# Optimization experiments

Measured on AMD Instinct MI355X. Metric: run time of the kernel, lower is better.

Reference implementation:

```python
import jax, jax.numpy as jnp
import numpy as np

B, L, D = 4, 2048, 1024
H, DK, DV = 16, 64, 64
EPS = 1e-6


def setup_inputs() -> dict:
    key = jax.random.key(0)
    ks = jax.random.split(key, 8)
    s = 0.02
    return {
        "q": jax.random.normal(ks[0], (B, L, D), dtype=jnp.float32),
        "k": jax.random.normal(ks[1], (B, L, D), dtype=jnp.float32),
        "v": jax.random.normal(ks[2], (B, L, D), dtype=jnp.float32),
        "Wq": jax.random.normal(ks[3], (H * DK, D), dtype=jnp.float32) * s,
        "Wk": jax.random.normal(ks[4], (H * DK, D), dtype=jnp.float32) * s,
        "Wv": jax.random.normal(ks[5], (H * DV, D), dtype=jnp.float32) * s,
        "Wfc": jax.random.normal(ks[6], (D, H * DV), dtype=jnp.float32) * s,
        "ln_g": jnp.ones((D,), dtype=jnp.float32),
        "ln_b": jnp.zeros((D,), dtype=jnp.float32),
    }


def reference(q, k, v, Wq, Wk, Wv, Wfc, ln_g, ln_b):
    residual = q
    # projections (Linear: x @ W.T), reshape to [B, H, L, d]
    qh = (q @ Wq.T).reshape(B, L, H, DK).transpose(0, 2, 1, 3)
    kh = (k @ Wk.T).reshape(B, L, H, DK).transpose(0, 2, 1, 3)
    vh = (v @ Wv.T).reshape(B, L, H, DV).transpose(0, 2, 1, 3)
    temperature = jnp.float32(DK) ** 0.5
    # scores [B, H, Lq, Lk]
    scores = jnp.einsum("bhqd,bhkd->bhqk", qh / temperature, kh)
    attn = jax.nn.softmax(scores, axis=-1)
    ctx = jnp.einsum("bhqk,bhkd->bhqd", attn, vh)  # [B, H, L, DV]
    ctx = ctx.transpose(0, 2, 1, 3).reshape(B, L, H * DV)
    out = ctx @ Wfc.T + residual
    # LayerNorm(eps=1e-6)
    mu = jnp.mean(out, axis=-1, keepdims=True)
    var = jnp.var(out, axis=-1, keepdims=True)
    out = (out - mu) * jax.lax.rsqrt(var + EPS) * ln_g + ln_b
    return out, attn
```

## Files before the change

### kernel.cpp

```cpp
#include <hip/hip_runtime.h>
#include <hip/hip_bf16.h>

typedef __bf16 bf16;
typedef __bf16 bf16x8 __attribute__((ext_vector_type(8)));
typedef __bf16 bf16x4 __attribute__((ext_vector_type(4)));
typedef __bf16 bf16x2 __attribute__((ext_vector_type(2)));
typedef float f32x4 __attribute__((ext_vector_type(4)));
typedef float f32x16 __attribute__((ext_vector_type(16)));
typedef unsigned int u32x4 __attribute__((ext_vector_type(4)));

#define MFMA_BF16(a, b, c) __builtin_amdgcn_mfma_f32_16x16x32_bf16((a), (b), (c), 0, 0, 0)
#define MFMA32(a, b, c) __builtin_amdgcn_mfma_f32_32x32x16_bf16((a), (b), (c), 0, 0, 0)

#if defined(__has_builtin)
#if __has_builtin(__builtin_amdgcn_exp2f)
#define EXP2F(x) __builtin_amdgcn_exp2f(x)
#endif
#endif
#ifndef EXP2F
#define EXP2F(x) exp2f(x)
#endif

static constexpr int Bc = 4, Lc = 2048, Dc = 1024, Hc = 16, DKc = 64;
static constexpr int BLc = Bc * Lc;
static constexpr float CEXP = 0.18033688011112042f;

__device__ inline unsigned pk2(float a, float b) {
  bf16x2 t;
  t[0] = (bf16)a;
  t[1] = (bf16)b;
  return __builtin_bit_cast(unsigned, t);
}

__global__ __launch_bounds__(256) void cvt_all(const float* __restrict__ s0,
                                               const float* __restrict__ s1,
                                               const float* __restrict__ s2,
                                               const float* __restrict__ s3,
                                               bf16* __restrict__ dst) {
  size_t i = ((size_t)blockIdx.x * 256 + threadIdx.x) * 8;
  const float* srcs[4] = {s0, s1, s2, s3};
  const float* sp = srcs[i >> 20] + (i & 1048575);
  float4 f0 = ((const float4*)sp)[0];
  float4 f1 = ((const float4*)sp)[1];
  bf16x8 o;
  o[0] = (bf16)f0.x; o[1] = (bf16)f0.y; o[2] = (bf16)f0.z; o[3] = (bf16)f0.w;
  o[4] = (bf16)f1.x; o[5] = (bf16)f1.y; o[6] = (bf16)f1.z; o[7] = (bf16)f1.w;
  *(bf16x8*)(dst + i) = o;
}

__global__ __launch_bounds__(256) void qkv_gemm(const float* __restrict__ qin,
                                                const float* __restrict__ kin,
                                                const float* __restrict__ vin,
                                                const bf16* __restrict__ Wb,
                                                bf16* __restrict__ qh,
                                                bf16* __restrict__ kh,
                                                bf16* __restrict__ vt) {
  __shared__ bf16 As[128][72];
  __shared__ bf16 Bs[128][72];
  const int t = threadIdx.x;
  const int lane = t & 63, wid = t >> 6;
  const int wr = wid >> 1, wc = wid & 1;
  const int which = blockIdx.y >> 3;
  const int m0 = blockIdx.x * 128, n0 = (blockIdx.y & 7) * 128;
  const float* A = which == 0 ? qin : which == 1 ? kin : vin;
  const bf16* Bw = Wb + ((size_t)which << 20);
  const int sub = t & 7, srow = t >> 3;

  f32x4 acc[4][4] = {};

  for (int kt = 0; kt < 1024; kt += 64) {
#pragma unroll
    for (int s = 0; s < 4; ++s) {
      int r = srow + 32 * s;
      const float4* pa = (const float4*)(A + (size_t)(m0 + r) * 1024 + kt + sub * 8);
      float4 f0 = pa[0], f1 = pa[1];
      bf16x8 o;
      o[0] = (bf16)f0.x; o[1] = (bf16)f0.y; o[2] = (bf16)f0.z; o[3] = (bf16)f0.w;
      o[4] = (bf16)f1.x; o[5] = (bf16)f1.y; o[6] = (bf16)f1.z; o[7] = (bf16)f1.w;
      *(bf16x8*)&As[r][sub * 8] = o;
    }
#pragma unroll
    for (int s = 0; s < 4; ++s) {
      int r = srow + 32 * s;
      u32x4 u = *(const u32x4*)(Bw + (size_t)(n0 + r) * 1024 + kt + sub * 8);
      *(u32x4*)&Bs[r][sub * 8] = u;
    }
    __syncthreads();
#pragma unroll
    for (int c = 0; c < 2; ++c) {
      const int ko = c * 32 + (lane >> 4) * 8;
      bf16x8 af[4], bfr[4];
#pragma unroll
      for (int m = 0; m < 4; ++m)
        af[m] = *(const bf16x8*)&As[wr * 64 + m * 16 + (lane & 15)][ko];
#pragma unroll
      for (int n = 0; n < 4; ++n)
        bfr[n] = *(const bf16x8*)&Bs[wc * 64 + n * 16 + (lane & 15)][ko];
#pragma unroll
      for (int m = 0; m < 4; ++m)
#pragma unroll
        for (int n = 0; n < 4; ++n)
          acc[m][n] = MFMA_BF16(af[m], bfr[n], acc[m][n]);
    }
    __syncthreads();
  }

  const int rbase = m0 + wr * 64 + (lane >> 4) * 4;
  const int cbase = n0 + wc * 64 + (lane & 15);
  if (which < 2) {
    bf16* C = which == 0 ? qh : kh;
#pragma unroll
    for (int m = 0; m < 4; ++m)
#pragma unroll
      for (int n = 0; n < 4; ++n)
#pragma unroll
        for (int r = 0; r < 4; ++r) {
          size_t row = (size_t)(rbase + m * 16 + r);
          size_t col = (size_t)(cbase + n * 16);
          C[row * 1024 + col] = (bf16)acc[m][n][r];
        }
  } else {
#pragma unroll
    for (int m = 0; m < 4; ++m)
#pragma unroll
      for (int n = 0; n < 4; ++n) {
        int row = rbase + m * 16;
        int col = cbase + n * 16;
        bf16x4 o;
#pragma unroll
        for (int r = 0; r < 4; ++r) o[r] = (bf16)acc[m][n][r];
        size_t dst = ((size_t)((row >> 11) << 10) + col) * 2048 + (row & 2047);
        *(bf16x4*)(vt + dst) = o;
      }
  }
}

__global__ __launch_bounds__(256) void fc_gemm(const bf16* __restrict__ A,
                                               const bf16* __restrict__ Bw,
                                               float* __restrict__ C,
                                               const float* __restrict__ resid) {
  __shared__ bf16 As[128][72];
  __shared__ bf16 Bs[128][72];
  const int t = threadIdx.x;
  const int lane = t & 63, wid = t >> 6;
  const int wr = wid >> 1, wc = wid & 1;
  const int m0 = blockIdx.x * 128, n0 = blockIdx.y * 128;
  const int sub = t & 7, srow = t >> 3;

  f32x4 acc[4][4] = {};

  for (int kt = 0; kt < 1024; kt += 64) {
#pragma unroll
    for (int s = 0; s < 4; ++s) {
      int r = srow + 32 * s;
      u32x4 u = *(const u32x4*)(A + (size_t)(m0 + r) * 1024 + kt + sub * 8);
      *(u32x4*)&As[r][sub * 8] = u;
    }
#pragma unroll
    for (int s = 0; s < 4; ++s) {
      int r = srow + 32 * s;
      u32x4 u = *(const u32x4*)(Bw + (size_t)(n0 + r) * 1024 + kt + sub * 8);
      *(u32x4*)&Bs[r][sub * 8] = u;
    }
    __syncthreads();
#pragma unroll
    for (int c = 0; c < 2; ++c) {
      const int ko = c * 32 + (lane >> 4) * 8;
      bf16x8 af[4], bfr[4];
#pragma unroll
      for (int m = 0; m < 4; ++m)
        af[m] = *(const bf16x8*)&As[wr * 64 + m * 16 + (lane & 15)][ko];
#pragma unroll
      for (int n = 0; n < 4; ++n)
        bfr[n] = *(const bf16x8*)&Bs[wc * 64 + n * 16 + (lane & 15)][ko];
#pragma unroll
      for (int m = 0; m < 4; ++m)
#pragma unroll
        for (int n = 0; n < 4; ++n)
          acc[m][n] = MFMA_BF16(af[m], bfr[n], acc[m][n]);
    }
    __syncthreads();
  }

  const int rbase = m0 + wr * 64 + (lane >> 4) * 4;
  const int cbase = n0 + wc * 64 + (lane & 15);
#pragma unroll
  for (int m = 0; m < 4; ++m)
#pragma unroll
    for (int n = 0; n < 4; ++n)
#pragma unroll
      for (int r = 0; r < 4; ++r) {
        size_t row = (size_t)(rbase + m * 16 + r);
        size_t col = (size_t)(cbase + n * 16);
        C[row * 1024 + col] = acc[m][n][r] + resid[row * 1024 + col];
      }
}

__global__ __launch_bounds__(256, 3) void attn_kernel(const bf16* __restrict__ qh,
                                                      const bf16* __restrict__ kh,
                                                      const bf16* __restrict__ vt,
                                                      bf16* __restrict__ ctx,
                                                      float* __restrict__ attn_out) {
  __shared__ bf16 Ks[64][72];
  __shared__ bf16 Vs[64][72];
  const int t = threadIdx.x, lane = t & 63, w = t >> 6;
  const int hi = lane >> 5, ql = lane & 31;
  const int qt = blockIdx.x, h = blockIdx.y, b = blockIdx.z;
  const size_t rowbase = (size_t)b * 2048;
  const int qrow = qt * 128 + w * 32 + ql;
  const bf16* kbase = kh + rowbase * 1024 + h * 64;
  const bf16* vbase = vt + (size_t)(b * 16 + h) * 64 * 2048;
  const int sub = t & 7, srow = t >> 3;

  bf16x8 qf[4];
  {
    const bf16* qp = qh + (rowbase + qrow) * 1024 + h * 64 + hi * 8;
#pragma unroll
    for (int c = 0; c < 4; ++c) qf[c] = *(const bf16x8*)(qp + c * 16);
  }

  f32x16 cacc[2] = {};
  float zacc = 0.f;

  for (int kt = 0; kt < 2048; kt += 64) {
    __syncthreads();
#pragma unroll
    for (int s = 0; s < 2; ++s) {
      int r = srow + 32 * s;
      *(u32x4*)&Ks[r][sub * 8] =
          *(const u32x4*)(kbase + (size_t)(kt + r) * 1024 + sub * 8);
      *(u32x4*)&Vs[r][sub * 8] =
          *(const u32x4*)(vbase + (size_t)r * 2048 + kt + sub * 8);
    }
    __syncthreads();
#pragma unroll
    for (int sb = 0; sb < 2; ++sb) {
      f32x16 s = {};
#pragma unroll
      for (int c = 0; c < 4; ++c) {
        bf16x8 kf = *(const bf16x8*)&Ks[sb * 32 + ql][c * 16 + hi * 8];
        s = MFMA32(kf, qf[c], s);
      }
      float p[16];
#pragma unroll
      for (int j = 0; j < 16; ++j) {
        p[j] = EXP2F(s[j] * CEXP);
        zacc += p[j];
      }
      unsigned pv[4][2];
#pragma unroll
      for (int o = 0; o < 4; ++o)
#pragma unroll
        for (int d = 0; d < 2; ++d) pv[o][d] = pk2(p[o * 4 + 2 * d], p[o * 4 + 2 * d + 1]);
      bf16x8 pa[2];
#pragma unroll
      for (int c = 0; c < 2; ++c) {
        u32x4 pu;
#pragma unroll
        for (int d = 0; d < 2; ++d) {
          unsigned a = pv[2 * c][d], bq = pv[2 * c + 1][d];
          unsigned as = (unsigned)__shfl_xor((int)a, 32);
          unsigned bs = (unsigned)__shfl_xor((int)bq, 32);
          pu[d] = hi ? bs : a;
          pu[2 + d] = hi ? bq : as;
        }
        pa[c] = __builtin_bit_cast(bf16x8, pu);
      }
#pragma unroll
      for (int n = 0; n < 2; ++n)
#pragma unroll
        for (int c = 0; c < 2; ++c) {
          bf16x8 vf = *(const bf16x8*)&Vs[n * 32 + ql][sb * 32 + c * 16 + hi * 8];
          cacc[n] = MFMA32(pa[c], vf, cacc[n]);
        }
    }
  }

  float z = zacc + __shfl_xor(zacc, 32);
  float rz = 1.0f / z;

  {
    float rzv[16];
#pragma unroll
    for (int g = 0; g < 16; ++g)
      rzv[g] = __shfl(rz, (g & 3) + 8 * (g >> 2) + 4 * hi);
#pragma unroll
    for (int n = 0; n < 2; ++n)
#pragma unroll
      for (int g = 0; g < 16; ++g) {
        int crow = (g & 3) + 8 * (g >> 2) + 4 * hi;
        size_t row = rowbase + (size_t)(qt * 128 + w * 32 + crow);
        ctx[row * 1024 + h * 64 + n * 32 + ql] = (bf16)(cacc[n][g] * rzv[g]);
      }
  }

  float* abase = attn_out + ((size_t)(b * 16 + h) * 2048 + qrow) * 2048;
  for (int kt = 0; kt < 2048; kt += 128) {
    __syncthreads();
#pragma unroll
    for (int s = 0; s < 2; ++s) {
      int r = srow + 32 * s;
      *(u32x4*)&Ks[r][sub * 8] =
          *(const u32x4*)(kbase + (size_t)(kt + r) * 1024 + sub * 8);
      *(u32x4*)&Vs[r][sub * 8] =
          *(const u32x4*)(kbase + (size_t)(kt + 64 + r) * 1024 + sub * 8);
    }
    __syncthreads();
#pragma unroll
    for (int half = 0; half < 2; ++half) {
      const bf16(*Kb)[72] = half ? Vs : Ks;
      const int kbase_off = kt + half * 64;
#pragma unroll
      for (int sb = 0; sb < 2; ++sb) {
        f32x16 s = {};
#pragma unroll
        for (int c = 0; c < 4; ++c) {
          bf16x8 kf = *(const bf16x8*)&Kb[sb * 32 + ql][c * 16 + hi * 8];
          s = MFMA32(kf, qf[c], s);
        }
#pragma unroll
        for (int o = 0; o < 4; ++o) {
          float4 v4;
          v4.x = EXP2F(s[o * 4 + 0] * CEXP) * rz;
          v4.y = EXP2F(s[o * 4 + 1] * CEXP) * rz;
          v4.z = EXP2F(s[o * 4 + 2] * CEXP) * rz;
          v4.w = EXP2F(s[o * 4 + 3] * CEXP) * rz;
          *(float4*)(abase + kbase_off + sb * 32 + o * 8 + hi * 4) = v4;
        }
      }
    }
  }
}

__global__ __launch_bounds__(256) void ln_kernel(float* __restrict__ io,
                                                 const float* __restrict__ g,
                                                 const float* __restrict__ bta) {
  const int row = blockIdx.x, t = threadIdx.x;
  float4* rp = (float4*)(io + (size_t)row * 1024);
  float4 v = rp[t];
  float s = v.x + v.y + v.z + v.w;
  float s2 = v.x * v.x + v.y * v.y + v.z * v.z + v.w * v.w;
#pragma unroll
  for (int off = 32; off >= 1; off >>= 1) {
    s += __shfl_xor(s, off);
    s2 += __shfl_xor(s2, off);
  }
  __shared__ float ls[4], ls2[4];
  const int w = t >> 6;
  if ((t & 63) == 0) { ls[w] = s; ls2[w] = s2; }
  __syncthreads();
  s = ls[0] + ls[1] + ls[2] + ls[3];
  s2 = ls2[0] + ls2[1] + ls2[2] + ls2[3];
  float mu = s * (1.f / 1024.f);
  float var = s2 * (1.f / 1024.f) - mu * mu;
  float rs = rsqrtf(var + 1e-6f);
  float4 gv = ((const float4*)g)[t];
  float4 bv = ((const float4*)bta)[t];
  v.x = (v.x - mu) * rs * gv.x + bv.x;
  v.y = (v.y - mu) * rs * gv.y + bv.y;
  v.z = (v.z - mu) * rs * gv.z + bv.z;
  v.w = (v.w - mu) * rs * gv.w + bv.w;
  rp[t] = v;
}

extern "C" void kernel_launch(void* const* d_in, const int* in_sizes, int n_in,
                              void* d_out, int out_size, void* d_ws, size_t ws_size,
                              hipStream_t stream) {
  (void)in_sizes; (void)n_in; (void)out_size; (void)ws_size;
  const float* q    = (const float*)d_in[0];
  const float* k    = (const float*)d_in[1];
  const float* v    = (const float*)d_in[2];
  const float* Wq   = (const float*)d_in[3];
  const float* Wk   = (const float*)d_in[4];
  const float* Wv   = (const float*)d_in[5];
  const float* Wfc  = (const float*)d_in[6];
  const float* ln_g = (const float*)d_in[7];
  const float* ln_b = (const float*)d_in[8];

  char* ws = (char*)d_ws;
  const size_t MB = 1024ull * 1024ull;
  bf16* wall = (bf16*)(ws + 0 * MB);
  bf16* wfcb = (bf16*)(ws + 6 * MB);
  bf16* qh   = (bf16*)(ws + 8 * MB);
  bf16* kh   = (bf16*)(ws + 24 * MB);
  bf16* vt   = (bf16*)(ws + 40 * MB);
  bf16* ctx  = (bf16*)(ws + 56 * MB);

  float* outp  = (float*)d_out;
  float* attnp = outp + (size_t)BLc * Dc;

  cvt_all<<<2048, 256, 0, stream>>>(Wq, Wk, Wv, Wfc, wall);

  qkv_gemm<<<dim3(64, 24), 256, 0, stream>>>(q, k, v, wall, qh, kh, vt);

  attn_kernel<<<dim3(16, 16, 4), 256, 0, stream>>>(qh, kh, vt, ctx, attnp);

  fc_gemm<<<dim3(64, 8), 256, 0, stream>>>(ctx, wfcb, outp, q);
  ln_kernel<<<8192, 256, 0, stream>>>(outp, ln_g, ln_b);
}
```

Before: 480.5 us.

## Double-buffer K/V tiles in attention pass and widen attn-write tile

The first attention pass now prefetches the next K/V tile into registers while computing on the current shared-memory buffer. This removes one barrier per iteration and hides global-load latency. The second pass, which writes the probabilities, now stages 256 keys per barrier pair across the doubled LDS. Launch bounds rise to 4 blocks per CU, which may add register pressure or spills given the extra prefetch registers and doubled LDS.

```diff
diff --git a/kernel.cpp b/kernel.cpp
--- a/kernel.cpp
+++ b/kernel.cpp
@@ -196,13 +196,13 @@
       }
 }
 
-__global__ __launch_bounds__(256, 3) void attn_kernel(const bf16* __restrict__ qh,
+__global__ __launch_bounds__(256, 4) void attn_kernel(const bf16* __restrict__ qh,
                                                       const bf16* __restrict__ kh,
                                                       const bf16* __restrict__ vt,
                                                       bf16* __restrict__ ctx,
                                                       float* __restrict__ attn_out) {
-  __shared__ bf16 Ks[64][72];
-  __shared__ bf16 Vs[64][72];
+  __shared__ bf16 Ks[2][64][72];
+  __shared__ bf16 Vs[2][64][72];
   const int t = threadIdx.x, lane = t & 63, w = t >> 6;
   const int hi = lane >> 5, ql = lane & 31;
   const int qt = blockIdx.x, h = blockIdx.y, b = blockIdx.z;
@@ -221,37 +221,48 @@
 
   f32x16 cacc[2] = {};
   float zacc = 0.f;
-
+  u32x4 kr0, kr1, vr0, vr1;
+
+#define LOADT(kt)                                                               \
+  {                                                                             \
+    kr0 = *(const u32x4*)(kbase + (size_t)((kt) + srow) * 1024 + sub * 8);      \
+    kr1 = *(const u32x4*)(kbase + (size_t)((kt) + srow + 32) * 1024 + sub * 8); \
+    vr0 = *(const u32x4*)(vbase + (size_t)srow * 2048 + (kt) + sub * 8);        \
+    vr1 = *(const u32x4*)(vbase + (size_t)(srow + 32) * 2048 + (kt) + sub * 8); \
+  }
+#define WRITET(bf)                                                              \
+  {                                                                             \
+    *(u32x4*)&Ks[bf][srow][sub * 8] = kr0;                                      \
+    *(u32x4*)&Ks[bf][srow + 32][sub * 8] = kr1;                                 \
+    *(u32x4*)&Vs[bf][srow][sub * 8] = vr0;                                      \
+    *(u32x4*)&Vs[bf][srow + 32][sub * 8] = vr1;                                 \
+  }
+
+  LOADT(0);
+  WRITET(0);
+  __syncthreads();
+  int buf = 0;
   for (int kt = 0; kt < 2048; kt += 64) {
-    __syncthreads();
-#pragma unroll
-    for (int s = 0; s < 2; ++s) {
-      int r = srow + 32 * s;
-      *(u32x4*)&Ks[r][sub * 8] =
-          *(const u32x4*)(kbase + (size_t)(kt + r) * 1024 + sub * 8);
-      *(u32x4*)&Vs[r][sub * 8] =
-          *(const u32x4*)(vbase + (size_t)r * 2048 + kt + sub * 8);
-    }
-    __syncthreads();
+    const bool notlast = kt + 64 < 2048;
+    if (notlast) LOADT(kt + 64);
 #pragma unroll
     for (int sb = 0; sb < 2; ++sb) {
       f32x16 s = {};
 #pragma unroll
       for (int c = 0; c < 4; ++c) {
-        bf16x8 kf = *(const bf16x8*)&Ks[sb * 32 + ql][c * 16 + hi * 8];
+        bf16x8 kf = *(const bf16x8*)&Ks[buf][sb * 32 + ql][c * 16 + hi * 8];
         s = MFMA32(kf, qf[c], s);
       }
-      float p[16];
-#pragma unroll
-      for (int j = 0; j < 16; ++j) {
-        p[j] = EXP2F(s[j] * CEXP);
-        zacc += p[j];
-      }
       unsigned pv[4][2];
 #pragma unroll
       for (int o = 0; o < 4; ++o)
 #pragma unroll
-        for (int d = 0; d < 2; ++d) pv[o][d] = pk2(p[o * 4 + 2 * d], p[o * 4 + 2 * d + 1]);
+        for (int d = 0; d < 2; ++d) {
+          float e0 = EXP2F(s[o * 4 + 2 * d] * CEXP);
+          float e1 = EXP2F(s[o * 4 + 2 * d + 1] * CEXP);
+          zacc += e0 + e1;
+          pv[o][d] = pk2(e0, e1);
+        }
       bf16x8 pa[2];
 #pragma unroll
       for (int c = 0; c < 2; ++c) {
@@ -270,11 +281,18 @@
       for (int n = 0; n < 2; ++n)
 #pragma unroll
         for (int c = 0; c < 2; ++c) {
-          bf16x8 vf = *(const bf16x8*)&Vs[n * 32 + ql][sb * 32 + c * 16 + hi * 8];
+          bf16x8 vf = *(const bf16x8*)&Vs[buf][n * 32 + ql][sb * 32 + c * 16 + hi * 8];
           cacc[n] = MFMA32(pa[c], vf, cacc[n]);
         }
     }
-  }
+    if (notlast) {
+      WRITET(buf ^ 1);
+      __syncthreads();
+      buf ^= 1;
+    }
+  }
+#undef LOADT
+#undef WRITET
 
   float z = zacc + __shfl_xor(zacc, 32);
   float rz = 1.0f / z;
@@ -295,27 +313,29 @@
   }
 
   float* abase = attn_out + ((size_t)(b * 16 + h) * 2048 + qrow) * 2048;
-  for (int kt = 0; kt < 2048; kt += 128) {
-    __syncthreads();
-#pragma unroll
-    for (int s = 0; s < 2; ++s) {
-      int r = srow + 32 * s;
-      *(u32x4*)&Ks[r][sub * 8] =
-          *(const u32x4*)(kbase + (size_t)(kt + r) * 1024 + sub * 8);
-      *(u32x4*)&Vs[r][sub * 8] =
-          *(const u32x4*)(kbase + (size_t)(kt + 64 + r) * 1024 + sub * 8);
-    }
-    __syncthreads();
-#pragma unroll
-    for (int half = 0; half < 2; ++half) {
-      const bf16(*Kb)[72] = half ? Vs : Ks;
-      const int kbase_off = kt + half * 64;
+  for (int kt = 0; kt < 2048; kt += 256) {
+    __syncthreads();
+#pragma unroll
+    for (int c4 = 0; c4 < 4; ++c4) {
+      bf16(*KB)[72] = c4 == 0 ? Ks[0] : c4 == 1 ? Ks[1] : c4 == 2 ? Vs[0] : Vs[1];
+#pragma unroll
+      for (int s = 0; s < 2; ++s) {
+        int r = srow + 32 * s;
+        *(u32x4*)&KB[r][sub * 8] =
+            *(const u32x4*)(kbase + (size_t)(kt + c4 * 64 + r) * 1024 + sub * 8);
+      }
+    }
+    __syncthreads();
+#pragma unroll
+    for (int c4 = 0; c4 < 4; ++c4) {
+      const bf16(*KB)[72] = c4 == 0 ? Ks[0] : c4 == 1 ? Ks[1] : c4 == 2 ? Vs[0] : Vs[1];
+      const int koff = kt + c4 * 64;
 #pragma unroll
       for (int sb = 0; sb < 2; ++sb) {
         f32x16 s = {};
 #pragma unroll
         for (int c = 0; c < 4; ++c) {
-          bf16x8 kf = *(const bf16x8*)&Kb[sb * 32 + ql][c * 16 + hi * 8];
+          bf16x8 kf = *(const bf16x8*)&KB[sb * 32 + ql][c * 16 + hi * 8];
           s = MFMA32(kf, qf[c], s);
         }
 #pragma unroll
@@ -325,7 +345,7 @@
           v4.y = EXP2F(s[o * 4 + 1] * CEXP) * rz;
           v4.z = EXP2F(s[o * 4 + 2] * CEXP) * rz;
           v4.w = EXP2F(s[o * 4 + 3] * CEXP) * rz;
-          *(float4*)(abase + kbase_off + sb * 32 + o * 8 + hi * 4) = v4;
+          *(float4*)(abase + koff + sb * 32 + o * 8 + hi * 4) = v4;
         }
       }
     }
```

Result: slower. 591.3 us (+23.1%).
